# Kernel tuning notes

Hardware: AMD Instinct MI355X
Metric: run time of the kernel (lower is better)

The kernel has to match this reference:

```python
import jax, jax.numpy as jnp
import numpy as np
from jax.scipy.special import logsumexp

T = 8192        # trajectory length
S_DIM = 256     # state feature dim
B_OPT = 64      # number of options b
N_ACT = 64      # number of actions
STOP_IX = 0     # STOP_NET_STOP_IX
CONT_IX = 1     # STOP_NET_CONTINUE_IX


def setup_inputs() -> dict:
    key = jax.random.key(0)
    k1, k2, k3, k4, k5 = jax.random.split(key, 5)
    s_i = jax.random.normal(k1, (T + 1, S_DIM), dtype=jnp.float32)
    W_action = jax.random.normal(k2, (S_DIM, B_OPT, N_ACT), dtype=jnp.float32) * 0.02
    W_stop = jax.random.normal(k3, (S_DIM, B_OPT, 2), dtype=jnp.float32) * 0.02
    W_start = jax.random.normal(k4, (S_DIM, B_OPT), dtype=jnp.float32) * 0.02
    actions = jax.random.randint(k5, (T,), 0, N_ACT, dtype=jnp.int32)
    return {"s_i": s_i, "W_action": W_action, "W_stop": W_stop,
            "W_start": W_start, "actions": actions, "lengths": T}


def reference(s_i, W_action, W_stop, W_start, actions, lengths):
    # control_net heads: per-state, per-option log-probabilities
    action_logps = jax.nn.log_softmax(jnp.einsum('ts,sbn->tbn', s_i, W_action), axis=-1)  # (T+1, b, n_act)
    stop_logps = jax.nn.log_softmax(jnp.einsum('ts,sbc->tbc', s_i, W_stop), axis=-1)      # (T+1, b, 2)
    start_logps = jax.nn.log_softmax(jnp.einsum('ts,sb->tb', s_i, W_start), axis=-1)      # (T+1, b)

    Tn = actions.shape[0]
    # emission logp of the taken action at each step: (T, b)
    emit = jnp.take_along_axis(action_logps[:Tn], actions[:, None, None].astype(jnp.int32), axis=2)[:, :, 0]

    f0 = start_logps[0] + emit[0]  # (b,)
    eye = jnp.eye(B_OPT, dtype=bool)
    neg_inf = jnp.float32(-jnp.inf)

    def step(f_prev, xs):
        beta, one_minus_beta, start, em = xs
        # trans[i, j] = logaddexp(beta_i + start_j, delta_ij * log(1-beta_i))
        cont = jnp.where(eye, one_minus_beta[:, None], neg_inf)
        trans = jnp.logaddexp(beta[:, None] + start[None, :], cont)
        f = logsumexp(f_prev[:, None] + trans + em[None, :], axis=0)
        return f, None

    xs = (stop_logps[1:Tn, :, STOP_IX], stop_logps[1:Tn, :, CONT_IX],
          start_logps[1:Tn], emit[1:])
    f, _ = jax.lax.scan(step, f0, xs)

    total_logp = logsumexp(f + stop_logps[Tn, :, STOP_IX])
    return -total_logp
```

## Files before the change

kernel.cpp:

```cpp
#include <hip/hip_runtime.h>
#include <stdint.h>


typedef short bf16x8 __attribute__((ext_vector_type(8)));
typedef float f32x4  __attribute__((ext_vector_type(4)));
typedef unsigned short u16;

#define T_LEN 8192
#define SDIM  256

#define WS_SBF    0
#define WS_WAT    4227072
#define WS_WSMT   6324224
#define WS_PE     6422528
#define WS_PS     8519680
#define WS_PB     10617088
#define WS_PC     12714496
#define WS_MOUT   14811904
#define WS_LSC    16909056
#define WS_GOUT   WS_PC
#define WS_GLSC   (WS_PC + 262144)

__device__ inline u16 f2bf(float f) {
  union { float f; uint32_t u; } v; v.f = f;
  uint32_t u = v.u;
  return (u16)((u + 0x7fffu + ((u >> 16) & 1u)) >> 16);
}

__global__ void conv_all(const float* __restrict__ s_i, const float* __restrict__ Wa,
                         const float* __restrict__ Wstop, const float* __restrict__ Wstart,
                         u16* __restrict__ s_bf, u16* __restrict__ wa_t,
                         u16* __restrict__ wsm_t) {
  __shared__ u16 tile[64 * 65];
  const int bid = blockIdx.x;
  const int tid = threadIdx.x;
  if (bid < 2064) {
    int idx = (bid * 256 + tid) * 4;
    int t = idx >> 8;
    ushort4 o;
    if (t < T_LEN + 1) {
      float4 v = *(const float4*)(s_i + idx);
      o = make_ushort4(f2bf(v.x), f2bf(v.y), f2bf(v.z), f2bf(v.w));
    } else {
      o = make_ushort4(0, 0, 0, 0);
    }
    *(ushort4*)(s_bf + idx) = o;
  } else if (bid < 2320) {
    int tb = bid - 2064;
    int s0 = (tb >> 6) * 64;
    int bn0 = (tb & 63) * 64;
#pragma unroll
    for (int it = 0; it < 16; ++it) {
      int i = tid + 256 * it;
      int r = i >> 6, cc = i & 63;
      tile[r * 65 + cc] = f2bf(Wa[(size_t)(s0 + r) * 4096 + bn0 + cc]);
    }
    __syncthreads();
#pragma unroll
    for (int it = 0; it < 16; ++it) {
      int i = tid + 256 * it;
      int r = i >> 6, cc = i & 63;
      wa_t[(size_t)(bn0 + r) * 256 + s0 + cc] = tile[cc * 65 + r];
    }
  } else {
    int idx = (bid - 2320) * 256 + tid;
    int col = idx >> 8, s = idx & 255;
    float v;
    if (col < 64)       v = Wstart[s * 64 + col];
    else if (col < 128) v = Wstop[s * 128 + (col - 64) * 2 + 0];
    else                v = Wstop[s * 128 + (col - 128) * 2 + 1];
    wsm_t[col * 256 + s] = f2bf(v);
  }
}

__global__ __launch_bounds__(256, 4) void gemm_fused(
    const u16* __restrict__ s_bf, const u16* __restrict__ wa_t,
    const u16* __restrict__ wsm_t, const int* __restrict__ actions,
    float* __restrict__ peT, float* __restrict__ ps,
    float* __restrict__ pb, float* __restrict__ pc) {
  __shared__ uint4 ldsU[64 * 32];
  const int tid = threadIdx.x;
  const int lane = tid & 63;
  const int w = tid >> 6;
  const int g = lane >> 4, c = lane & 15;
  const int bid = blockIdx.x;

  if (bid < 129) {
    uint4* sA = ldsU;
    uint4* sB = ldsU + 512;
    const int t0 = bid * 64;

    f32x4 acc[12];
#pragma unroll
    for (int i = 0; i < 12; ++i) acc[i] = (f32x4){0.f, 0.f, 0.f, 0.f};

    for (int kq = 0; kq < 4; ++kq) {
      if (kq) __syncthreads();
#pragma unroll
      for (int i = tid; i < 512; i += 256) {
        int row = i >> 3, u = i & 7;
        sA[row * 8 + (u ^ (row & 7))] =
            *(const uint4*)(s_bf + (size_t)(t0 + row) * 256 + kq * 64 + u * 8);
      }
#pragma unroll
      for (int i = tid; i < 1536; i += 256) {
        int row = i >> 3, u = i & 7;
        sB[row * 8 + (u ^ (row & 7))] =
            *(const uint4*)(wsm_t + (size_t)row * 256 + kq * 64 + u * 8);
      }
      __syncthreads();
#pragma unroll
      for (int kk = 0; kk < 2; ++kk) {
        int u = kk * 4 + g;
        int arow = w * 16 + c;
        bf16x8 af = *(const bf16x8*)&sA[arow * 8 + (u ^ (arow & 7))];
#pragma unroll
        for (int cf = 0; cf < 12; ++cf) {
          int brow = cf * 16 + c;
          bf16x8 bfr = *(const bf16x8*)&sB[brow * 8 + (u ^ (brow & 7))];
          acc[cf] = __builtin_amdgcn_mfma_f32_16x16x32_bf16(af, bfr, acc[cf], 0, 0, 0);
        }
      }
    }

#pragma unroll
    for (int q = 0; q < 4; ++q) {
      int t = t0 + w * 16 + g * 4 + q;
      float v0 = acc[0][q], v1 = acc[1][q], v2 = acc[2][q], v3 = acc[3][q];
      float m = fmaxf(fmaxf(v0, v1), fmaxf(v2, v3));
#pragma unroll
      for (int d = 1; d < 16; d <<= 1) m = fmaxf(m, __shfl_xor(m, d));
      float s = __expf(v0 - m) + __expf(v1 - m) + __expf(v2 - m) + __expf(v3 - m);
#pragma unroll
      for (int d = 1; d < 16; d <<= 1) s += __shfl_xor(s, d);
      float lse = m + __logf(s);
      if (t <= T_LEN) {
        ps[t * 64 + 0 * 16 + c] = __expf(v0 - lse);
        ps[t * 64 + 1 * 16 + c] = __expf(v1 - lse);
        ps[t * 64 + 2 * 16 + c] = __expf(v2 - lse);
        ps[t * 64 + 3 * 16 + c] = __expf(v3 - lse);
#pragma unroll
        for (int bf = 0; bf < 4; ++bf) {
          float l0 = acc[4 + bf][q], l1 = acc[8 + bf][q];
          float d01 = l0 - l1;
          pb[t * 64 + bf * 16 + c] = 1.f / (1.f + __expf(-d01));
          pc[t * 64 + bf * 16 + c] = 1.f / (1.f + __expf(d01));
        }
      }
    }
    return;
  }

  const int abid = bid - 129;
  int swz = (abid & 7) * 512 + (abid >> 3);
  const int t0 = (swz >> 6) * 128;
  const int b0 = swz & 63;
  const int tbase = t0 + w * 32;

  int act[2][4];
#pragma unroll
  for (int mf = 0; mf < 2; ++mf)
#pragma unroll
    for (int q = 0; q < 4; ++q)
      act[mf][q] = actions[tbase + mf * 16 + g * 4 + q];

  const u16* aRow0 = s_bf + (size_t)(tbase + c) * 256;
  const u16* aRow1 = s_bf + (size_t)(tbase + 16 + c) * 256;

  bf16x8 af0[2][4];
#pragma unroll
  for (int ks = 0; ks < 4; ++ks) {
    af0[0][ks] = *(const bf16x8*)(aRow0 + ks * 32 + g * 8);
    af0[1][ks] = *(const bf16x8*)(aRow1 + ks * 32 + g * 8);
  }

  {
    const u16* bsrc = wa_t + (size_t)b0 * 64 * 256;
#pragma unroll
    for (int it = 0; it < 8; ++it) {
      int i = tid + 256 * it;
      int r = i >> 5, s = i & 31;
      ldsU[r * 32 + (s ^ (r & 7))] = *(const uint4*)(bsrc + r * 256 + s * 8);
    }
  }
  __syncthreads();

  f32x4 acc[2][4];
#pragma unroll
  for (int mf = 0; mf < 2; ++mf)
#pragma unroll
    for (int nf = 0; nf < 4; ++nf) acc[mf][nf] = (f32x4){0.f, 0.f, 0.f, 0.f};

  bf16x8 af1[2][4];
#pragma unroll
  for (int ks = 0; ks < 4; ++ks) {
    af1[0][ks] = *(const bf16x8*)(aRow0 + 128 + ks * 32 + g * 8);
    af1[1][ks] = *(const bf16x8*)(aRow1 + 128 + ks * 32 + g * 8);
  }

#pragma unroll
  for (int ks = 0; ks < 4; ++ks) {
#pragma unroll
    for (int nf = 0; nf < 4; ++nf) {
      int rr = nf * 16 + c;
      bf16x8 bfv = *(const bf16x8*)&ldsU[rr * 32 + ((ks * 4 + g) ^ (rr & 7))];
      acc[0][nf] = __builtin_amdgcn_mfma_f32_16x16x32_bf16(af0[0][ks], bfv, acc[0][nf], 0, 0, 0);
      acc[1][nf] = __builtin_amdgcn_mfma_f32_16x16x32_bf16(af0[1][ks], bfv, acc[1][nf], 0, 0, 0);
    }
  }
#pragma unroll
  for (int ks = 0; ks < 4; ++ks) {
#pragma unroll
    for (int nf = 0; nf < 4; ++nf) {
      int rr = nf * 16 + c;
      bf16x8 bfv = *(const bf16x8*)&ldsU[rr * 32 + (((ks + 4) * 4 + g) ^ (rr & 7))];
      acc[0][nf] = __builtin_amdgcn_mfma_f32_16x16x32_bf16(af1[0][ks], bfv, acc[0][nf], 0, 0, 0);
      acc[1][nf] = __builtin_amdgcn_mfma_f32_16x16x32_bf16(af1[1][ks], bfv, acc[1][nf], 0, 0, 0);
    }
  }

  const size_t pebase = (size_t)b0 * 8192;
#pragma unroll
  for (int mf = 0; mf < 2; ++mf) {
#pragma unroll
    for (int q = 0; q < 4; ++q) {
      float e0 = __expf(acc[mf][0][q]);
      float e1 = __expf(acc[mf][1][q]);
      float e2 = __expf(acc[mf][2][q]);
      float e3 = __expf(acc[mf][3][q]);
      float s = (e0 + e1) + (e2 + e3);
#pragma unroll
      for (int d = 1; d < 16; d <<= 1) s += __shfl_xor(s, d);
      int a = act[mf][q];
      int acf = a >> 4;
      float esel = (acf == 0) ? e0 : (acf == 1) ? e1 : (acf == 2) ? e2 : e3;
      if (c == (a & 15))
        peT[pebase + tbase + mf * 16 + g * 4 + q] = esel / s;
    }
  }
}

__global__ __launch_bounds__(256) void chunk_kernel(
    const float* __restrict__ peT, const float* __restrict__ ps,
    const float* __restrict__ pb, const float* __restrict__ pc,
    float* __restrict__ Mout, float* __restrict__ lscale) {
  __shared__ float scal[64 * 196];
  __shared__ float mxs[4];
  const int ck = blockIdx.x;
  const int tid = threadIdx.x;
  const int lane = tid & 63;
  const int w = tid >> 6;
  const int tlo = ck * 64 + 1;

#pragma unroll
  for (int it = 0; it < 16; ++it) {
    int i = tid + 256 * it;
    int st = i >> 6, j = i & 63;
    int t = tlo + st;
    if (t <= T_LEN - 1) {
      int base = t * 64 + j;
      scal[st * 196 + j]       = pb[base];
      scal[st * 196 + 64 + j]  = pc[base];
      scal[st * 196 + 128 + j] = ps[base];
    } else {
      scal[st * 196 + j]       = 0.f;
      scal[st * 196 + 64 + j]  = 1.f;
      scal[st * 196 + 128 + j] = 0.f;
    }
  }
  __syncthreads();
#pragma unroll
  for (int it = 0; it < 16; ++it) {
    int i = tid + 256 * it;
    int j = i >> 6, st = i & 63;
    int t = tlo + st;
    if (t <= T_LEN - 1) {
      float e = peT[(size_t)j * 8192 + t];
      scal[st * 196 + 64 + j]  *= e;
      scal[st * 196 + 128 + j] *= e;
    }
  }
  __syncthreads();

  const int kcol = w * 16 + (lane >> 2);
  const int roff = (lane & 3) * 16;

  float M[16];
#pragma unroll
  for (int jj = 0; jj < 16; ++jj) M[jj] = ((roff + jj) == kcol) ? 1.f : 0.f;
  float lsc = 0.f;

  for (int st8 = 0; st8 < 8; ++st8) {
#pragma unroll
    for (int s8 = 0; s8 < 8; ++s8) {
      const float* sb = &scal[(st8 * 8 + s8) * 196];
      float4 b0 = *(const float4*)(sb + roff + 0);
      float4 b1 = *(const float4*)(sb + roff + 4);
      float4 b2 = *(const float4*)(sb + roff + 8);
      float4 b3 = *(const float4*)(sb + roff + 12);
      float p0 = 0.f, p1 = 0.f, p2 = 0.f, p3 = 0.f;
      p0 = fmaf(b0.x, M[0], p0);  p1 = fmaf(b0.y, M[1], p1);
      p2 = fmaf(b0.z, M[2], p2);  p3 = fmaf(b0.w, M[3], p3);
      p0 = fmaf(b1.x, M[4], p0);  p1 = fmaf(b1.y, M[5], p1);
      p2 = fmaf(b1.z, M[6], p2);  p3 = fmaf(b1.w, M[7], p3);
      p0 = fmaf(b2.x, M[8], p0);  p1 = fmaf(b2.y, M[9], p1);
      p2 = fmaf(b2.z, M[10], p2); p3 = fmaf(b2.w, M[11], p3);
      p0 = fmaf(b3.x, M[12], p0); p1 = fmaf(b3.y, M[13], p1);
      p2 = fmaf(b3.z, M[14], p2); p3 = fmaf(b3.w, M[15], p3);
      float p = (p0 + p1) + (p2 + p3);
      p += __shfl_xor(p, 1);
      p += __shfl_xor(p, 2);
      float4 e0 = *(const float4*)(sb + 64 + roff + 0);
      float4 e1 = *(const float4*)(sb + 64 + roff + 4);
      float4 e2 = *(const float4*)(sb + 64 + roff + 8);
      float4 e3 = *(const float4*)(sb + 64 + roff + 12);
      float4 s0 = *(const float4*)(sb + 128 + roff + 0);
      float4 s1 = *(const float4*)(sb + 128 + roff + 4);
      float4 s2 = *(const float4*)(sb + 128 + roff + 8);
      float4 s3 = *(const float4*)(sb + 128 + roff + 12);
      M[0]  = fmaf(e0.x, M[0],  s0.x * p);  M[1]  = fmaf(e0.y, M[1],  s0.y * p);
      M[2]  = fmaf(e0.z, M[2],  s0.z * p);  M[3]  = fmaf(e0.w, M[3],  s0.w * p);
      M[4]  = fmaf(e1.x, M[4],  s1.x * p);  M[5]  = fmaf(e1.y, M[5],  s1.y * p);
      M[6]  = fmaf(e1.z, M[6],  s1.z * p);  M[7]  = fmaf(e1.w, M[7],  s1.w * p);
      M[8]  = fmaf(e2.x, M[8],  s2.x * p);  M[9]  = fmaf(e2.y, M[9],  s2.y * p);
      M[10] = fmaf(e2.z, M[10], s2.z * p);  M[11] = fmaf(e2.w, M[11], s2.w * p);
      M[12] = fmaf(e3.x, M[12], s3.x * p);  M[13] = fmaf(e3.y, M[13], s3.y * p);
      M[14] = fmaf(e3.z, M[14], s3.z * p);  M[15] = fmaf(e3.w, M[15], s3.w * p);
    }
    float mx = M[0];
#pragma unroll
    for (int jj = 1; jj < 16; ++jj) mx = fmaxf(mx, M[jj]);
#pragma unroll
    for (int d = 1; d < 64; d <<= 1) mx = fmaxf(mx, __shfl_xor(mx, d));
    if (lane == 0) mxs[w] = mx;
    __syncthreads();
    float bm = fmaxf(fmaxf(mxs[0], mxs[1]), fmaxf(mxs[2], mxs[3]));
    float inv = 1.f / bm;
#pragma unroll
    for (int jj = 0; jj < 16; ++jj) M[jj] *= inv;
    lsc += __logf(bm);
    __syncthreads();
  }

  float* out = Mout + (size_t)ck * 4096 + kcol * 64 + roff;
  *(float4*)(out + 0)  = make_float4(M[0],  M[1],  M[2],  M[3]);
  *(float4*)(out + 4)  = make_float4(M[4],  M[5],  M[6],  M[7]);
  *(float4*)(out + 8)  = make_float4(M[8],  M[9],  M[10], M[11]);
  *(float4*)(out + 12) = make_float4(M[12], M[13], M[14], M[15]);
  if (tid == 0) lscale[ck] = lsc;
}

__global__ __launch_bounds__(256) void group_combine(
    const float* __restrict__ Mout, const float* __restrict__ lscale,
    float* __restrict__ Gout, float* __restrict__ glsc) {
  const int g = blockIdx.x;
  const int tid = threadIdx.x;
  const int j = tid & 63;
  const int w = tid >> 6;
  __shared__ float Xa[64 * 68];
  __shared__ float Xb[64 * 68];
  __shared__ float Ma[64 * 68];
  __shared__ float Mb[64 * 68];
  __shared__ float red[4];

  {
    const float* M0 = Mout + (size_t)(8 * g) * 4096;
    const float* M1 = Mout + (size_t)(8 * g + 1) * 4096;
    for (int idx = tid; idx < 4096; idx += 256) {
      int i = idx >> 6, r = idx & 63;
      Xa[r * 68 + i] = M0[idx];
      Ma[i * 68 + r] = M1[idx];
    }
  }
  __syncthreads();

  float lsc = 0.f;
  float* Xcur = Xa; float* Xnxt = Xb;
  float* Mcur = Ma; float* Mnxt = Mb;

  for (int m = 1; m < 8; ++m) {
    float4 pf[4];
    if (m < 7) {
      const float* Mn = Mout + (size_t)(8 * g + m + 1) * 4096;
#pragma unroll
      for (int ii = 0; ii < 4; ++ii)
        pf[ii] = *(const float4*)(Mn + tid * 4 + 1024 * ii);
    }

    float acc[16];
#pragma unroll
    for (int i = 0; i < 16; ++i) acc[i] = 0.f;

#pragma unroll 4
    for (int k = 0; k < 64; ++k) {
      float mv = Mcur[k * 68 + j];
      const float* xr = Xcur + k * 68 + (w << 4);
      float4 x0 = *(const float4*)(xr + 0);
      float4 x1 = *(const float4*)(xr + 4);
      float4 x2 = *(const float4*)(xr + 8);
      float4 x3 = *(const float4*)(xr + 12);
      acc[0]  = fmaf(mv, x0.x, acc[0]);  acc[1]  = fmaf(mv, x0.y, acc[1]);
      acc[2]  = fmaf(mv, x0.z, acc[2]);  acc[3]  = fmaf(mv, x0.w, acc[3]);
      acc[4]  = fmaf(mv, x1.x, acc[4]);  acc[5]  = fmaf(mv, x1.y, acc[5]);
      acc[6]  = fmaf(mv, x1.z, acc[6]);  acc[7]  = fmaf(mv, x1.w, acc[7]);
      acc[8]  = fmaf(mv, x2.x, acc[8]);  acc[9]  = fmaf(mv, x2.y, acc[9]);
      acc[10] = fmaf(mv, x2.z, acc[10]); acc[11] = fmaf(mv, x2.w, acc[11]);
      acc[12] = fmaf(mv, x3.x, acc[12]); acc[13] = fmaf(mv, x3.y, acc[13]);
      acc[14] = fmaf(mv, x3.z, acc[14]); acc[15] = fmaf(mv, x3.w, acc[15]);
    }

    float lm = acc[0];
#pragma unroll
    for (int i = 1; i < 16; ++i) lm = fmaxf(lm, acc[i]);
#pragma unroll
    for (int d = 1; d < 64; d <<= 1) lm = fmaxf(lm, __shfl_xor(lm, d));
    if ((tid & 63) == 0) red[w] = lm;
    __syncthreads();
    float bm = fmaxf(fmaxf(red[0], red[1]), fmaxf(red[2], red[3]));
    float inv = 1.f / bm;
    lsc += __logf(bm);
#pragma unroll
    for (int i = 0; i < 16; ++i)
      Xnxt[j * 68 + (w << 4) + i] = acc[i] * inv;
    if (m < 7) {
#pragma unroll
      for (int ii = 0; ii < 4; ++ii) {
        int idx = tid * 4 + 1024 * ii;
        int k = idx >> 6, jj = idx & 63;
        *(float4*)(Mnxt + k * 68 + jj) = pf[ii];
      }
    }
    __syncthreads();
    float* t = Xcur; Xcur = Xnxt; Xnxt = t;
    float* tm = Mcur; Mcur = Mnxt; Mnxt = tm;
  }

  float* out = Gout + (size_t)g * 4096;
  for (int idx = tid; idx < 4096; idx += 256) {
    int i = idx >> 6, r = idx & 63;
    out[idx] = Xcur[r * 68 + i];
  }
  if (tid == 0) {
    float s = lsc;
#pragma unroll
    for (int m = 0; m < 8; ++m) s += lscale[8 * g + m];
    glsc[g] = s;
  }
}

__global__ __launch_bounds__(256) void final_combine(
    const float* __restrict__ Gout, const float* __restrict__ glsc,
    const float* __restrict__ peT, const float* __restrict__ ps,
    const float* __restrict__ pb, float* __restrict__ out) {
  const int tid = threadIdx.x;
  const int j = tid & 63, w = tid >> 6;
  __shared__ float vsh[64];
  __shared__ float part[4 * 64];
  if (tid < 64) vsh[tid] = ps[tid] * peT[(size_t)tid * 8192];
  __syncthreads();
  double lsc = 0.0;
  for (int gph = 0; gph < 16; ++gph) {
    const float* Gc = Gout + (size_t)gph * 4096;
    const int k0 = w << 4;
    float a0 = 0.f, a1 = 0.f, a2 = 0.f, a3 = 0.f;
#pragma unroll
    for (int kk = 0; kk < 16; kk += 4) {
      a0 = fmaf(vsh[k0 + kk + 0], Gc[(k0 + kk + 0) * 64 + j], a0);
      a1 = fmaf(vsh[k0 + kk + 1], Gc[(k0 + kk + 1) * 64 + j], a1);
      a2 = fmaf(vsh[k0 + kk + 2], Gc[(k0 + kk + 2) * 64 + j], a2);
      a3 = fmaf(vsh[k0 + kk + 3], Gc[(k0 + kk + 3) * 64 + j], a3);
    }
    part[w * 64 + j] = (a0 + a1) + (a2 + a3);
    __syncthreads();
    if (w == 0) {
      float u = part[j] + part[64 + j] + part[128 + j] + part[192 + j];
      float mx = u;
#pragma unroll
      for (int d = 1; d < 64; d <<= 1) mx = fmaxf(mx, __shfl_xor(mx, d));
      vsh[j] = u / mx;
      lsc += (double)__logf(mx) + (double)glsc[gph];
    }
    __syncthreads();
  }
  if (w == 0) {
    float z = vsh[j] * pb[T_LEN * 64 + j];
#pragma unroll
    for (int d = 1; d < 64; d <<= 1) z += __shfl_xor(z, d);
    if (j == 0) out[0] = (float)(-((double)logf(z) + lsc));
  }
}

extern "C" void kernel_launch(void* const* d_in, const int* in_sizes, int n_in,
                              void* d_out, int out_size, void* d_ws, size_t ws_size,
                              hipStream_t stream) {
  const float* s_i      = (const float*)d_in[0];
  const float* W_action = (const float*)d_in[1];
  const float* W_stop   = (const float*)d_in[2];
  const float* W_start  = (const float*)d_in[3];
  const int*   actions  = (const int*)d_in[4];

  char* ws = (char*)d_ws;
  u16*   s_bf  = (u16*)(ws + WS_SBF);
  u16*   wa_t  = (u16*)(ws + WS_WAT);
  u16*   wsm_t = (u16*)(ws + WS_WSMT);
  float* peT   = (float*)(ws + WS_PE);
  float* ps    = (float*)(ws + WS_PS);
  float* pb    = (float*)(ws + WS_PB);
  float* pc    = (float*)(ws + WS_PC);
  float* Mout  = (float*)(ws + WS_MOUT);
  float* lsc   = (float*)(ws + WS_LSC);
  float* Gout  = (float*)(ws + WS_GOUT);
  float* glsc  = (float*)(ws + WS_GLSC);

  conv_all<<<2512, 256, 0, stream>>>(s_i, W_action, W_stop, W_start, s_bf, wa_t, wsm_t);
  gemm_fused<<<4225, 256, 0, stream>>>(s_bf, wa_t, wsm_t, actions, peT, ps, pb, pc);
  chunk_kernel<<<128, 256, 0, stream>>>(peT, ps, pb, pc, Mout, lsc);
  group_combine<<<16, 256, 0, stream>>>(Mout, lsc, Gout, glsc);
  final_combine<<<1, 256, 0, stream>>>(Gout, glsc, peT, ps, pb, (float*)d_out);
}
```

Before: 126.0 us.

## Fuse chunk, group and final scan stages into one kernel with atomic flags

Merges the three scan-phase kernels (chunk products, group combine, final combine) into a single launch. Blocks signal completion through atomic counters, and the first 16 blocks and then block 0 spin-wait on them before doing the later stages. Flags are zeroed by an extra block in the conversion kernel. This removes two kernel launches and their gaps. It relies on all 128 blocks being co-resident to avoid deadlock, and it shares one shared-memory buffer across the stages.

New measurement: 143.2 us. +13.6%, slower.

```diff
diff --git a/kernel.cpp b/kernel.cpp
--- a/kernel.cpp
+++ b/kernel.cpp
@@ -20,6 +20,7 @@
 #define WS_LSC    16909056
 #define WS_GOUT   WS_PC
 #define WS_GLSC   (WS_PC + 262144)
+#define WS_FLAGS  16910080
 
 __device__ inline u16 f2bf(float f) {
   union { float f; uint32_t u; } v; v.f = f;
@@ -30,7 +31,7 @@
 __global__ void conv_all(const float* __restrict__ s_i, const float* __restrict__ Wa,
                          const float* __restrict__ Wstop, const float* __restrict__ Wstart,
                          u16* __restrict__ s_bf, u16* __restrict__ wa_t,
-                         u16* __restrict__ wsm_t) {
+                         u16* __restrict__ wsm_t, unsigned* __restrict__ flags) {
   __shared__ u16 tile[64 * 65];
   const int bid = blockIdx.x;
   const int tid = threadIdx.x;
@@ -62,7 +63,7 @@
       int r = i >> 6, cc = i & 63;
       wa_t[(size_t)(bn0 + r) * 256 + s0 + cc] = tile[cc * 65 + r];
     }
-  } else {
+  } else if (bid < 2512) {
     int idx = (bid - 2320) * 256 + tid;
     int col = idx >> 8, s = idx & 255;
     float v;
@@ -70,6 +71,8 @@
     else if (col < 128) v = Wstop[s * 128 + (col - 64) * 2 + 0];
     else                v = Wstop[s * 128 + (col - 128) * 2 + 1];
     wsm_t[col * 256 + s] = f2bf(v);
+  } else {
+    if (tid < 17) flags[tid] = 0u;
   }
 }
 
@@ -240,253 +243,269 @@
   }
 }
 
-__global__ __launch_bounds__(256) void chunk_kernel(
+__global__ __launch_bounds__(256) void scan_all(
     const float* __restrict__ peT, const float* __restrict__ ps,
     const float* __restrict__ pb, const float* __restrict__ pc,
-    float* __restrict__ Mout, float* __restrict__ lscale) {
-  __shared__ float scal[64 * 196];
-  __shared__ float mxs[4];
+    float* __restrict__ Mout, float* __restrict__ lscale,
+    float* __restrict__ Gout, float* __restrict__ glsc,
+    unsigned* __restrict__ flags, float* __restrict__ out) {
+  __shared__ float smem[13072];
   const int ck = blockIdx.x;
   const int tid = threadIdx.x;
   const int lane = tid & 63;
   const int w = tid >> 6;
-  const int tlo = ck * 64 + 1;
-
-#pragma unroll
-  for (int it = 0; it < 16; ++it) {
-    int i = tid + 256 * it;
-    int st = i >> 6, j = i & 63;
-    int t = tlo + st;
-    if (t <= T_LEN - 1) {
-      int base = t * 64 + j;
-      scal[st * 196 + j]       = pb[base];
-      scal[st * 196 + 64 + j]  = pc[base];
-      scal[st * 196 + 128 + j] = ps[base];
-    } else {
-      scal[st * 196 + j]       = 0.f;
-      scal[st * 196 + 64 + j]  = 1.f;
-      scal[st * 196 + 128 + j] = 0.f;
-    }
-  }
+
+  {
+    float* scal = smem;
+    float* mxs  = smem + 12544;
+    const int tlo = ck * 64 + 1;
+
+#pragma unroll
+    for (int it = 0; it < 16; ++it) {
+      int i = tid + 256 * it;
+      int st = i >> 6, j = i & 63;
+      int t = tlo + st;
+      if (t <= T_LEN - 1) {
+        int base = t * 64 + j;
+        scal[st * 196 + j]       = pb[base];
+        scal[st * 196 + 64 + j]  = pc[base];
+        scal[st * 196 + 128 + j] = ps[base];
+      } else {
+        scal[st * 196 + j]       = 0.f;
+        scal[st * 196 + 64 + j]  = 1.f;
+        scal[st * 196 + 128 + j] = 0.f;
+      }
+    }
+    __syncthreads();
+#pragma unroll
+    for (int it = 0; it < 16; ++it) {
+      int i = tid + 256 * it;
+      int j = i >> 6, st = i & 63;
+      int t = tlo + st;
+      if (t <= T_LEN - 1) {
+        float e = peT[(size_t)j * 8192 + t];
+        scal[st * 196 + 64 + j]  *= e;
+        scal[st * 196 + 128 + j] *= e;
+      }
+    }
+    __syncthreads();
+
+    const int kcol = w * 16 + (lane >> 2);
+    const int roff = (lane & 3) * 16;
+
+    float M[16];
+#pragma unroll
+    for (int jj = 0; jj < 16; ++jj) M[jj] = ((roff + jj) == kcol) ? 1.f : 0.f;
+    float lsc = 0.f;
+
+    for (int st8 = 0; st8 < 8; ++st8) {
+#pragma unroll
+      for (int s8 = 0; s8 < 8; ++s8) {
+        const float* sb = &scal[(st8 * 8 + s8) * 196];
+        float4 b0 = *(const float4*)(sb + roff + 0);
+        float4 b1 = *(const float4*)(sb + roff + 4);
+        float4 b2 = *(const float4*)(sb + roff + 8);
+        float4 b3 = *(const float4*)(sb + roff + 12);
+        float p0 = 0.f, p1 = 0.f, p2 = 0.f, p3 = 0.f;
+        p0 = fmaf(b0.x, M[0], p0);  p1 = fmaf(b0.y, M[1], p1);
+        p2 = fmaf(b0.z, M[2], p2);  p3 = fmaf(b0.w, M[3], p3);
+        p0 = fmaf(b1.x, M[4], p0);  p1 = fmaf(b1.y, M[5], p1);
+        p2 = fmaf(b1.z, M[6], p2);  p3 = fmaf(b1.w, M[7], p3);
+        p0 = fmaf(b2.x, M[8], p0);  p1 = fmaf(b2.y, M[9], p1);
+        p2 = fmaf(b2.z, M[10], p2); p3 = fmaf(b2.w, M[11], p3);
+        p0 = fmaf(b3.x, M[12], p0); p1 = fmaf(b3.y, M[13], p1);
+        p2 = fmaf(b3.z, M[14], p2); p3 = fmaf(b3.w, M[15], p3);
+        float p = (p0 + p1) + (p2 + p3);
+        p += __shfl_xor(p, 1);
+        p += __shfl_xor(p, 2);
+        float4 e0 = *(const float4*)(sb + 64 + roff + 0);
+        float4 e1 = *(const float4*)(sb + 64 + roff + 4);
+        float4 e2 = *(const float4*)(sb + 64 + roff + 8);
+        float4 e3 = *(const float4*)(sb + 64 + roff + 12);
+        float4 s0 = *(const float4*)(sb + 128 + roff + 0);
+        float4 s1 = *(const float4*)(sb + 128 + roff + 4);
+        float4 s2 = *(const float4*)(sb + 128 + roff + 8);
+        float4 s3 = *(const float4*)(sb + 128 + roff + 12);
+        M[0]  = fmaf(e0.x, M[0],  s0.x * p);  M[1]  = fmaf(e0.y, M[1],  s0.y * p);
+        M[2]  = fmaf(e0.z, M[2],  s0.z * p);  M[3]  = fmaf(e0.w, M[3],  s0.w * p);
+        M[4]  = fmaf(e1.x, M[4],  s1.x * p);  M[5]  = fmaf(e1.y, M[5],  s1.y * p);
+        M[6]  = fmaf(e1.z, M[6],  s1.z * p);  M[7]  = fmaf(e1.w, M[7],  s1.w * p);
+        M[8]  = fmaf(e2.x, M[8],  s2.x * p);  M[9]  = fmaf(e2.y, M[9],  s2.y * p);
+        M[10] = fmaf(e2.z, M[10], s2.z * p);  M[11] = fmaf(e2.w, M[11], s2.w * p);
+        M[12] = fmaf(e3.x, M[12], s3.x * p);  M[13] = fmaf(e3.y, M[13], s3.y * p);
+        M[14] = fmaf(e3.z, M[14], s3.z * p);  M[15] = fmaf(e3.w, M[15], s3.w * p);
+      }
+      float mx = M[0];
+#pragma unroll
+      for (int jj = 1; jj < 16; ++jj) mx = fmaxf(mx, M[jj]);
+#pragma unroll
+      for (int d = 1; d < 64; d <<= 1) mx = fmaxf(mx, __shfl_xor(mx, d));
+      if (lane == 0) mxs[w] = mx;
+      __syncthreads();
+      float bm = fmaxf(fmaxf(mxs[0], mxs[1]), fmaxf(mxs[2], mxs[3]));
+      float inv = 1.f / bm;
+#pragma unroll
+      for (int jj = 0; jj < 16; ++jj) M[jj] *= inv;
+      lsc += __logf(bm);
+      __syncthreads();
+    }
+
+    float* o = Mout + (size_t)ck * 4096 + kcol * 64 + roff;
+    *(float4*)(o + 0)  = make_float4(M[0],  M[1],  M[2],  M[3]);
+    *(float4*)(o + 4)  = make_float4(M[4],  M[5],  M[6],  M[7]);
+    *(float4*)(o + 8)  = make_float4(M[8],  M[9],  M[10], M[11]);
+    *(float4*)(o + 12) = make_float4(M[12], M[13], M[14], M[15]);
+    if (tid == 0) lscale[ck] = lsc;
+  }
+  __threadfence();
   __syncthreads();
-#pragma unroll
-  for (int it = 0; it < 16; ++it) {
-    int i = tid + 256 * it;
-    int j = i >> 6, st = i & 63;
-    int t = tlo + st;
-    if (t <= T_LEN - 1) {
-      float e = peT[(size_t)j * 8192 + t];
-      scal[st * 196 + 64 + j]  *= e;
-      scal[st * 196 + 128 + j] *= e;
-    }
-  }
-  __syncthreads();
-
-  const int kcol = w * 16 + (lane >> 2);
-  const int roff = (lane & 3) * 16;
-
-  float M[16];
-#pragma unroll
-  for (int jj = 0; jj < 16; ++jj) M[jj] = ((roff + jj) == kcol) ? 1.f : 0.f;
-  float lsc = 0.f;
-
-  for (int st8 = 0; st8 < 8; ++st8) {
-#pragma unroll
-    for (int s8 = 0; s8 < 8; ++s8) {
-      const float* sb = &scal[(st8 * 8 + s8) * 196];
-      float4 b0 = *(const float4*)(sb + roff + 0);
-      float4 b1 = *(const float4*)(sb + roff + 4);
-      float4 b2 = *(const float4*)(sb + roff + 8);
-      float4 b3 = *(const float4*)(sb + roff + 12);
-      float p0 = 0.f, p1 = 0.f, p2 = 0.f, p3 = 0.f;
-      p0 = fmaf(b0.x, M[0], p0);  p1 = fmaf(b0.y, M[1], p1);
-      p2 = fmaf(b0.z, M[2], p2);  p3 = fmaf(b0.w, M[3], p3);
-      p0 = fmaf(b1.x, M[4], p0);  p1 = fmaf(b1.y, M[5], p1);
-      p2 = fmaf(b1.z, M[6], p2);  p3 = fmaf(b1.w, M[7], p3);
-      p0 = fmaf(b2.x, M[8], p0);  p1 = fmaf(b2.y, M[9], p1);
-      p2 = fmaf(b2.z, M[10], p2); p3 = fmaf(b2.w, M[11], p3);
-      p0 = fmaf(b3.x, M[12], p0); p1 = fmaf(b3.y, M[13], p1);
-      p2 = fmaf(b3.z, M[14], p2); p3 = fmaf(b3.w, M[15], p3);
-      float p = (p0 + p1) + (p2 + p3);
-      p += __shfl_xor(p, 1);
-      p += __shfl_xor(p, 2);
-      float4 e0 = *(const float4*)(sb + 64 + roff + 0);
-      float4 e1 = *(const float4*)(sb + 64 + roff + 4);
-      float4 e2 = *(const float4*)(sb + 64 + roff + 8);
-      float4 e3 = *(const float4*)(sb + 64 + roff + 12);
-      float4 s0 = *(const float4*)(sb + 128 + roff + 0);
-      float4 s1 = *(const float4*)(sb + 128 + roff + 4);
-      float4 s2 = *(const float4*)(sb + 128 + roff + 8);
-      float4 s3 = *(const float4*)(sb + 128 + roff + 12);
-      M[0]  = fmaf(e0.x, M[0],  s0.x * p);  M[1]  = fmaf(e0.y, M[1],  s0.y * p);
-      M[2]  = fmaf(e0.z, M[2],  s0.z * p);  M[3]  = fmaf(e0.w, M[3],  s0.w * p);
-      M[4]  = fmaf(e1.x, M[4],  s1.x * p);  M[5]  = fmaf(e1.y, M[5],  s1.y * p);
-      M[6]  = fmaf(e1.z, M[6],  s1.z * p);  M[7]  = fmaf(e1.w, M[7],  s1.w * p);
-      M[8]  = fmaf(e2.x, M[8],  s2.x * p);  M[9]  = fmaf(e2.y, M[9],  s2.y * p);
-      M[10] = fmaf(e2.z, M[10], s2.z * p);  M[11] = fmaf(e2.w, M[11], s2.w * p);
-      M[12] = fmaf(e3.x, M[12], s3.x * p);  M[13] = fmaf(e3.y, M[13], s3.y * p);
-      M[14] = fmaf(e3.z, M[14], s3.z * p);  M[15] = fmaf(e3.w, M[15], s3.w * p);
-    }
-    float mx = M[0];
-#pragma unroll
-    for (int jj = 1; jj < 16; ++jj) mx = fmaxf(mx, M[jj]);
-#pragma unroll
-    for (int d = 1; d < 64; d <<= 1) mx = fmaxf(mx, __shfl_xor(mx, d));
-    if (lane == 0) mxs[w] = mx;
-    __syncthreads();
-    float bm = fmaxf(fmaxf(mxs[0], mxs[1]), fmaxf(mxs[2], mxs[3]));
-    float inv = 1.f / bm;
-#pragma unroll
-    for (int jj = 0; jj < 16; ++jj) M[jj] *= inv;
-    lsc += __logf(bm);
-    __syncthreads();
-  }
-
-  float* out = Mout + (size_t)ck * 4096 + kcol * 64 + roff;
-  *(float4*)(out + 0)  = make_float4(M[0],  M[1],  M[2],  M[3]);
-  *(float4*)(out + 4)  = make_float4(M[4],  M[5],  M[6],  M[7]);
-  *(float4*)(out + 8)  = make_float4(M[8],  M[9],  M[10], M[11]);
-  *(float4*)(out + 12) = make_float4(M[12], M[13], M[14], M[15]);
-  if (tid == 0) lscale[ck] = lsc;
-}
-
-__global__ __launch_bounds__(256) void group_combine(
-    const float* __restrict__ Mout, const float* __restrict__ lscale,
-    float* __restrict__ Gout, float* __restrict__ glsc) {
-  const int g = blockIdx.x;
-  const int tid = threadIdx.x;
-  const int j = tid & 63;
-  const int w = tid >> 6;
-  __shared__ float Xa[64 * 68];
-  __shared__ float Xb[64 * 68];
-  __shared__ float Ma[64 * 68];
-  __shared__ float Mb[64 * 68];
-  __shared__ float red[4];
+  if (tid == 0) atomicAdd(&flags[ck >> 3], 1u);
+
+  if (ck >= 16) return;
 
   {
-    const float* M0 = Mout + (size_t)(8 * g) * 4096;
-    const float* M1 = Mout + (size_t)(8 * g + 1) * 4096;
+    const int g = ck;
+    if (tid == 0) {
+      while (atomicAdd(&flags[g], 0u) < 8u) __builtin_amdgcn_s_sleep(8);
+    }
+    __syncthreads();
+    __threadfence();
+
+    float* Xa  = smem;
+    float* Xb  = smem + 4352;
+    float* Mb  = smem + 8704;
+    float* red = smem + 13056;
+    {
+      const float* M0 = Mout + (size_t)(8 * g) * 4096;
+      const float* M1 = Mout + (size_t)(8 * g + 1) * 4096;
+      for (int idx = tid; idx < 4096; idx += 256) {
+        int i = idx >> 6, r = idx & 63;
+        Xa[r * 68 + i] = M0[idx];
+        Mb[i * 68 + r] = M1[idx];
+      }
+    }
+    __syncthreads();
+
+    float lsc = 0.f;
+    float* Xcur = Xa; float* Xnxt = Xb;
+    const int j = tid & 63;
+
+    for (int m = 1; m < 8; ++m) {
+      float4 pf[4];
+      if (m < 7) {
+        const float* Mn = Mout + (size_t)(8 * g + m + 1) * 4096;
+#pragma unroll
+        for (int ii = 0; ii < 4; ++ii)
+          pf[ii] = *(const float4*)(Mn + tid * 4 + 1024 * ii);
+      }
+
+      float acc[16];
+#pragma unroll
+      for (int i = 0; i < 16; ++i) acc[i] = 0.f;
+
+#pragma unroll 4
+      for (int k = 0; k < 64; ++k) {
+        float mv = Mb[k * 68 + j];
+        const float* xr = Xcur + k * 68 + (w << 4);
+        float4 x0 = *(const float4*)(xr + 0);
+        float4 x1 = *(const float4*)(xr + 4);
+        float4 x2 = *(const float4*)(xr + 8);
+        float4 x3 = *(const float4*)(xr + 12);
+        acc[0]  = fmaf(mv, x0.x, acc[0]);  acc[1]  = fmaf(mv, x0.y, acc[1]);
+        acc[2]  = fmaf(mv, x0.z, acc[2]);  acc[3]  = fmaf(mv, x0.w, acc[3]);
+        acc[4]  = fmaf(mv, x1.x, acc[4]);  acc[5]  = fmaf(mv, x1.y, acc[5]);
+        acc[6]  = fmaf(mv, x1.z, acc[6]);  acc[7]  = fmaf(mv, x1.w, acc[7]);
+        acc[8]  = fmaf(mv, x2.x, acc[8]);  acc[9]  = fmaf(mv, x2.y, acc[9]);
+        acc[10] = fmaf(mv, x2.z, acc[10]); acc[11] = fmaf(mv, x2.w, acc[11]);
+        acc[12] = fmaf(mv, x3.x, acc[12]); acc[13] = fmaf(mv, x3.y, acc[13]);
+        acc[14] = fmaf(mv, x3.z, acc[14]); acc[15] = fmaf(mv, x3.w, acc[15]);
+      }
+
+      float lm = acc[0];
+#pragma unroll
+      for (int i = 1; i < 16; ++i) lm = fmaxf(lm, acc[i]);
+#pragma unroll
+      for (int d = 1; d < 64; d <<= 1) lm = fmaxf(lm, __shfl_xor(lm, d));
+      if ((tid & 63) == 0) red[w] = lm;
+      __syncthreads();
+      float bm = fmaxf(fmaxf(red[0], red[1]), fmaxf(red[2], red[3]));
+      float inv = 1.f / bm;
+      lsc += __logf(bm);
+#pragma unroll
+      for (int i = 0; i < 16; ++i)
+        Xnxt[j * 68 + (w << 4) + i] = acc[i] * inv;
+      if (m < 7) {
+#pragma unroll
+        for (int ii = 0; ii < 4; ++ii) {
+          int idx = tid * 4 + 1024 * ii;
+          int k = idx >> 6, jj = idx & 63;
+          *(float4*)(Mb + k * 68 + jj) = pf[ii];
+        }
+      }
+      __syncthreads();
+      float* t = Xcur; Xcur = Xnxt; Xnxt = t;
+    }
+
+    float* og = Gout + (size_t)g * 4096;
     for (int idx = tid; idx < 4096; idx += 256) {
       int i = idx >> 6, r = idx & 63;
-      Xa[r * 68 + i] = M0[idx];
-      Ma[i * 68 + r] = M1[idx];
-    }
-  }
+      og[idx] = Xcur[r * 68 + i];
+    }
+    if (tid == 0) {
+      float s = lsc;
+#pragma unroll
+      for (int m = 0; m < 8; ++m) s += lscale[8 * g + m];
+      glsc[g] = s;
+    }
+  }
+  __threadfence();
   __syncthreads();
-
-  float lsc = 0.f;
-  float* Xcur = Xa; float* Xnxt = Xb;
-  float* Mcur = Ma; float* Mnxt = Mb;
-
-  for (int m = 1; m < 8; ++m) {
-    float4 pf[4];
-    if (m < 7) {
-      const float* Mn = Mout + (size_t)(8 * g + m + 1) * 4096;
-#pragma unroll
-      for (int ii = 0; ii < 4; ++ii)
-        pf[ii] = *(const float4*)(Mn + tid * 4 + 1024 * ii);
-    }
-
-    float acc[16];
-#pragma unroll
-    for (int i = 0; i < 16; ++i) acc[i] = 0.f;
-
-#pragma unroll 4
-    for (int k = 0; k < 64; ++k) {
-      float mv = Mcur[k * 68 + j];
-      const float* xr = Xcur + k * 68 + (w << 4);
-      float4 x0 = *(const float4*)(xr + 0);
-      float4 x1 = *(const float4*)(xr + 4);
-      float4 x2 = *(const float4*)(xr + 8);
-      float4 x3 = *(const float4*)(xr + 12);
-      acc[0]  = fmaf(mv, x0.x, acc[0]);  acc[1]  = fmaf(mv, x0.y, acc[1]);
-      acc[2]  = fmaf(mv, x0.z, acc[2]);  acc[3]  = fmaf(mv, x0.w, acc[3]);
-      acc[4]  = fmaf(mv, x1.x, acc[4]);  acc[5]  = fmaf(mv, x1.y, acc[5]);
-      acc[6]  = fmaf(mv, x1.z, acc[6]);  acc[7]  = fmaf(mv, x1.w, acc[7]);
-      acc[8]  = fmaf(mv, x2.x, acc[8]);  acc[9]  = fmaf(mv, x2.y, acc[9]);
-      acc[10] = fmaf(mv, x2.z, acc[10]); acc[11] = fmaf(mv, x2.w, acc[11]);
-      acc[12] = fmaf(mv, x3.x, acc[12]); acc[13] = fmaf(mv, x3.y, acc[13]);
-      acc[14] = fmaf(mv, x3.z, acc[14]); acc[15] = fmaf(mv, x3.w, acc[15]);
-    }
-
-    float lm = acc[0];
-#pragma unroll
-    for (int i = 1; i < 16; ++i) lm = fmaxf(lm, acc[i]);
-#pragma unroll
-    for (int d = 1; d < 64; d <<= 1) lm = fmaxf(lm, __shfl_xor(lm, d));
-    if ((tid & 63) == 0) red[w] = lm;
-    __syncthreads();
-    float bm = fmaxf(fmaxf(red[0], red[1]), fmaxf(red[2], red[3]));
-    float inv = 1.f / bm;
-    lsc += __logf(bm);
-#pragma unroll
-    for (int i = 0; i < 16; ++i)
-      Xnxt[j * 68 + (w << 4) + i] = acc[i] * inv;
-    if (m < 7) {
-#pragma unroll
-      for (int ii = 0; ii < 4; ++ii) {
-        int idx = tid * 4 + 1024 * ii;
-        int k = idx >> 6, jj = idx & 63;
-        *(float4*)(Mnxt + k * 68 + jj) = pf[ii];
-      }
-    }
-    __syncthreads();
-    float* t = Xcur; Xcur = Xnxt; Xnxt = t;
-    float* tm = Mcur; Mcur = Mnxt; Mnxt = tm;
-  }
-
-  float* out = Gout + (size_t)g * 4096;
-  for (int idx = tid; idx < 4096; idx += 256) {
-    int i = idx >> 6, r = idx & 63;
-    out[idx] = Xcur[r * 68 + i];
-  }
-  if (tid == 0) {
-    float s = lsc;
-#pragma unroll
-    for (int m = 0; m < 8; ++m) s += lscale[8 * g + m];
-    glsc[g] = s;
-  }
-}
-
-__global__ __launch_bounds__(256) void final_combine(
-    const float* __restrict__ Gout, const float* __restrict__ glsc,
-    const float* __restrict__ peT, const float* __restrict__ ps,
-    const float* __restrict__ pb, float* __restrict__ out) {
-  const int tid = threadIdx.x;
-  const int j = tid & 63, w = tid >> 6;
-  __shared__ float vsh[64];
-  __shared__ float part[4 * 64];
-  if (tid < 64) vsh[tid] = ps[tid] * peT[(size_t)tid * 8192];
-  __syncthreads();
-  double lsc = 0.0;
-  for (int gph = 0; gph < 16; ++gph) {
-    const float* Gc = Gout + (size_t)gph * 4096;
-    const int k0 = w << 4;
-    float a0 = 0.f, a1 = 0.f, a2 = 0.f, a3 = 0.f;
-#pragma unroll
-    for (int kk = 0; kk < 16; kk += 4) {
-      a0 = fmaf(vsh[k0 + kk + 0], Gc[(k0 + kk + 0) * 64 + j], a0);
-      a1 = fmaf(vsh[k0 + kk + 1], Gc[(k0 + kk + 1) * 64 + j], a1);
-      a2 = fmaf(vsh[k0 + kk + 2], Gc[(k0 + kk + 2) * 64 + j], a2);
-      a3 = fmaf(vsh[k0 + kk + 3], Gc[(k0 + kk + 3) * 64 + j], a3);
-    }
-    part[w * 64 + j] = (a0 + a1) + (a2 + a3);
-    __syncthreads();
+  if (tid == 0) atomicAdd(&flags[16], 1u);
+
+  if (ck != 0) return;
+
+  {
+    if (tid == 0) {
+      while (atomicAdd(&flags[16], 0u) < 16u) __builtin_amdgcn_s_sleep(8);
+    }
+    __syncthreads();
+    __threadfence();
+
+    float* vsh  = smem;
+    float* part = smem + 64;
+    const int j = tid & 63;
+    if (tid < 64) vsh[tid] = ps[tid] * peT[(size_t)tid * 8192];
+    __syncthreads();
+    double lsc = 0.0;
+    for (int gph = 0; gph < 16; ++gph) {
+      const float* Gc = Gout + (size_t)gph * 4096;
+      const int k0 = w << 4;
+      float a0 = 0.f, a1 = 0.f, a2 = 0.f, a3 = 0.f;
+#pragma unroll
+      for (int kk = 0; kk < 16; kk += 4) {
+        a0 = fmaf(vsh[k0 + kk + 0], Gc[(k0 + kk + 0) * 64 + j], a0);
+        a1 = fmaf(vsh[k0 + kk + 1], Gc[(k0 + kk + 1) * 64 + j], a1);
+        a2 = fmaf(vsh[k0 + kk + 2], Gc[(k0 + kk + 2) * 64 + j], a2);
+        a3 = fmaf(vsh[k0 + kk + 3], Gc[(k0 + kk + 3) * 64 + j], a3);
+      }
+      part[w * 64 + j] = (a0 + a1) + (a2 + a3);
+      __syncthreads();
+      if (w == 0) {
+        float u = part[j] + part[64 + j] + part[128 + j] + part[192 + j];
+        float mx = u;
+#pragma unroll
+        for (int d = 1; d < 64; d <<= 1) mx = fmaxf(mx, __shfl_xor(mx, d));
+        vsh[j] = u / mx;
+        lsc += (double)__logf(mx) + (double)glsc[gph];
+      }
+      __syncthreads();
+    }
     if (w == 0) {
-      float u = part[j] + part[64 + j] + part[128 + j] + part[192 + j];
-      float mx = u;
-#pragma unroll
-      for (int d = 1; d < 64; d <<= 1) mx = fmaxf(mx, __shfl_xor(mx, d));
-      vsh[j] = u / mx;
-      lsc += (double)__logf(mx) + (double)glsc[gph];
-    }
-    __syncthreads();
-  }
-  if (w == 0) {
-    float z = vsh[j] * pb[T_LEN * 64 + j];
-#pragma unroll
-    for (int d = 1; d < 64; d <<= 1) z += __shfl_xor(z, d);
-    if (j == 0) out[0] = (float)(-((double)logf(z) + lsc));
+      float z = vsh[j] * pb[T_LEN * 64 + j];
+#pragma unroll
+      for (int d = 1; d < 64; d <<= 1) z += __shfl_xor(z, d);
+      if (j == 0) out[0] = (float)(-((double)logf(z) + lsc));
+    }
   }
 }
 
@@ -511,10 +530,9 @@
   float* lsc   = (float*)(ws + WS_LSC);
   float* Gout  = (float*)(ws + WS_GOUT);
   float* glsc  = (float*)(ws + WS_GLSC);
-
-  conv_all<<<2512, 256, 0, stream>>>(s_i, W_action, W_stop, W_start, s_bf, wa_t, wsm_t);
+  unsigned* flags = (unsigned*)(ws + WS_FLAGS);
+
+  conv_all<<<2513, 256, 0, stream>>>(s_i, W_action, W_stop, W_start, s_bf, wa_t, wsm_t, flags);
   gemm_fused<<<4225, 256, 0, stream>>>(s_bf, wa_t, wsm_t, actions, peT, ps, pb, pc);
-  chunk_kernel<<<128, 256, 0, stream>>>(peT, ps, pb, pc, Mout, lsc);
-  group_combine<<<16, 256, 0, stream>>>(Mout, lsc, Gout, glsc);
-  final_combine<<<1, 256, 0, stream>>>(Gout, glsc, peT, ps, pb, (float*)d_out);
+  scan_all<<<128, 256, 0, stream>>>(peT, ps, pb, pc, Mout, lsc, Gout, glsc, flags, (float*)d_out);
 }
```
